# Optimization experiments

Measured on AMD Instinct MI355X. Metric: run time of the kernel, lower is better.

## Reference

```python
import jax, jax.numpy as jnp
import numpy as np

THRESH = 0.9   # config['thresh_cnn']
R = 2          # config['radius'] -> maxpool kernel 2R+1=5, stride 1, padding R


def setup_inputs() -> dict:
    key = jax.random.key(0)
    # [B=1, C=1, D=64, H=512, W=512]
    pred_vol = jax.random.uniform(key, (1, 1, 64, 512, 512), dtype=jnp.float32)
    return {"pred_vol": pred_vol}


def reference(pred_vol):
    # threshold: keep values > thresh, else 0
    pred_thresh = jnp.where(pred_vol > THRESH, pred_vol, 0.0)
    # 3D max-pool, kernel 2R+1, stride 1, padding R (torch pads with -inf for maxpool)
    k = 2 * R + 1
    mp = jax.lax.reduce_window(
        pred_thresh, -jnp.inf, jax.lax.max,
        window_dimensions=(1, 1, k, k, k),
        window_strides=(1, 1, 1, 1, 1),
        padding=[(0, 0), (0, 0), (R, R), (R, R), (R, R)],
    )
    # keep only strict local maxima of the thresholded volume
    conf_vol = jnp.where((mp > 0.0) & (mp == pred_thresh), mp, 0.0)
    return jnp.squeeze(conf_vol)  # [D, H, W] dense peak confidence map
```

## Files before the change

### kernel.cpp

```cpp
#include <hip/hip_runtime.h>


#define THRESH 0.9f

constexpr int D = 64, H = 512, W = 512;
constexpr int HW = H * W;
constexpr int TW = 64;
constexpr int TH = 16;
constexpr int DCHUNK = 16;
constexpr int HALO = 2;
constexpr int LROWS = TH + 2 * HALO;
constexpr int RAWQ  = TW / 4 + 2;
constexpr int RAW_S = RAWQ + 1;
constexpr int NS = DCHUNK + 2 * HALO;

typedef float floatx4 __attribute__((ext_vector_type(4)));

__device__ __forceinline__ void barrier_no_drain() {
    asm volatile("s_waitcnt lgkmcnt(0)\n\ts_barrier" ::: "memory");
}

__device__ __forceinline__ float4 max4(float4 a, float4 b) {
    return make_float4(fmaxf(a.x, b.x), fmaxf(a.y, b.y),
                       fmaxf(a.z, b.z), fmaxf(a.w, b.w));
}

__device__ __forceinline__ float4 wmax5s(float f2, float f3, float4 b,
                                         float f8, float f9) {
    const float f4 = b.x, f5 = b.y, f6 = b.z, f7 = b.w;
    const float m45 = fmaxf(f4, f5);
    const float m56 = fmaxf(f5, f6);
    const float m345 = fmaxf(f3, m45);
    const float m456 = fmaxf(f4, m56);
    const float m567 = fmaxf(m56, f7);
    const float m678 = fmaxf(fmaxf(f6, f7), f8);
    float4 r;
    r.x = fmaxf(fmaxf(f2, f6), m345);
    r.y = fmaxf(fmaxf(f3, f7), m456);
    r.z = fmaxf(fmaxf(f4, f8), m567);
    r.w = fmaxf(fmaxf(f5, f9), m678);
    return r;
}

__global__ __launch_bounds__(256)
void peak3d_kernel(const float* __restrict__ in, float* __restrict__ out) {
    __shared__ float4 raw[2][LROWS * RAW_S];

    const int tx = threadIdx.x;
    const int ty = threadIdx.y;
    const int tid = ty * 16 + tx;

    const int w0 = blockIdx.x * TW;
    const int h0 = blockIdx.y * TH;
    const int d0 = blockIdx.z * DCHUNK;

    const int q0 = tid;
    const int q1 = tid + 256;
    const int r0 = q0 / RAWQ, c0 = q0 % RAWQ;
    const int r1 = q1 / RAWQ, c1 = q1 % RAWQ;
    const int lds0 = r0 * RAW_S + c0;
    const int lds1 = r1 * RAW_S + c1;
    const int gh0 = h0 + r0 - HALO, gw0 = w0 + 4 * c0 - 4;
    const int gh1 = h0 + r1 - HALO, gw1 = w0 + 4 * c1 - 4;
    const bool has1 = (q1 < LROWS * RAWQ);
    const bool ib0 = (gh0 >= 0 && gh0 < H && gw0 >= 0 && gw0 < W);
    const bool ib1 = has1 && (gh1 >= 0 && gh1 < H && gw1 >= 0 && gw1 < W);
    const size_t off0 = ib0 ? ((size_t)gh0 * W + gw0) : 0;
    const size_t off1 = ib1 ? ((size_t)gh1 * W + gw1) : 0;

    const float4 zero4 = make_float4(0.f, 0.f, 0.f, 0.f);
    float4 win[5], cen[5];
#pragma unroll
    for (int k = 0; k < 5; ++k) { win[k] = zero4; cen[k] = zero4; }

    auto loadSlice = [&](int dd, float4& a, float4& b) {
        a = zero4; b = zero4;
        if (dd >= 0 && dd < D) {
            const size_t base = (size_t)dd * HW;
            if (ib0) a = *reinterpret_cast<const float4*>(in + base + off0);
            if (ib1) b = *reinterpret_cast<const float4*>(in + base + off1);
        }
    };

    float4 pfa[2], pfb[2];
    loadSlice(d0 - HALO + 0, pfa[0], pfb[0]);
    loadSlice(d0 - HALO + 1, pfa[1], pfb[1]);

    const int hcol = (tx == 0) ? 0 : (RAWQ - 1);

#pragma unroll
    for (int t = 0; t < NS; ++t) {
        const int buf = t & 1;

        raw[buf][lds0] = pfa[buf];
        if (has1) raw[buf][lds1] = pfb[buf];
        if (t + 2 < NS) loadSlice(d0 - HALO + t + 2, pfa[buf], pfb[buf]);

        barrier_no_drain();

        const float4* bp = &raw[buf][0];
        const float4 r0q = bp[(ty + 0) * RAW_S + (tx + 1)];
        const float4 r1q = bp[(ty + 1) * RAW_S + (tx + 1)];
        const float4 r2q = bp[(ty + 2) * RAW_S + (tx + 1)];
        const float4 r3q = bp[(ty + 3) * RAW_S + (tx + 1)];
        const float4 r4q = bp[(ty + 4) * RAW_S + (tx + 1)];
        const float4 hv = max4(max4(max4(r0q, r1q), max4(r3q, r4q)), r2q);

        const float4 e0 = bp[(ty + 0) * RAW_S + hcol];
        const float4 e1 = bp[(ty + 1) * RAW_S + hcol];
        const float4 e2 = bp[(ty + 2) * RAW_S + hcol];
        const float4 e3 = bp[(ty + 3) * RAW_S + hcol];
        const float4 e4 = bp[(ty + 4) * RAW_S + hcol];
        const float4 hq = max4(max4(max4(e0, e1), max4(e3, e4)), e2);

        float f2 = __shfl_up(hv.z, 1);
        float f3 = __shfl_up(hv.w, 1);
        float f8 = __shfl_down(hv.x, 1);
        float f9 = __shfl_down(hv.y, 1);
        if (tx == 0)  { f2 = hq.z; f3 = hq.w; }
        if (tx == 15) { f8 = hq.x; f9 = hq.y; }

        win[t % 5] = wmax5s(f2, f3, hv, f8, f9);
        cen[t % 5] = r2q;

        if (t >= 4) {
            const int dout = d0 + (t - 4);
            const float4 mp = max4(max4(max4(win[0], win[1]),
                                        max4(win[2], win[3])), win[4]);
            const float4 c = cen[(t + 3) % 5];
            floatx4 res;
            res.x = (c.x > THRESH && mp.x == c.x) ? c.x : 0.f;
            res.y = (c.y > THRESH && mp.y == c.y) ? c.y : 0.f;
            res.z = (c.z > THRESH && mp.z == c.z) ? c.z : 0.f;
            res.w = (c.w > THRESH && mp.w == c.w) ? c.w : 0.f;
            floatx4* op = reinterpret_cast<floatx4*>(
                out + (size_t)dout * HW + (size_t)(h0 + ty) * W + (w0 + 4 * tx));
            __builtin_nontemporal_store(res, op);
        }
    }
}

extern "C" void kernel_launch(void* const* d_in, const int* in_sizes, int n_in,
                              void* d_out, int out_size, void* d_ws, size_t ws_size,
                              hipStream_t stream) {
    const float* in = (const float*)d_in[0];
    float* out = (float*)d_out;
    dim3 grid(W / TW, H / TH, D / DCHUNK);
    dim3 block(16, 16, 1);
    hipLaunchKernelGGL(peak3d_kernel, grid, block, 0, stream, in, out);
}
```

Before: 116.6 us.

## Do W-direction max in registers before LDS, then vertical max from LDS

Each thread now loads three adjacent float4s per row (left, middle, right) straight from global memory and computes the 5-wide W max in registers. Only the W-maxed rows and the center values go to LDS, so the shuffles and separate halo-column reads are gone. The depth prefetch drops from two slices to one. This cuts LDS traffic and shuffle work but triples global load instructions, relying on cache hits for the overlapping neighbour reads, and raises register use.

```diff
diff --git a/kernel.cpp b/kernel.cpp
--- a/kernel.cpp
+++ b/kernel.cpp
@@ -10,8 +10,9 @@
 constexpr int DCHUNK = 16;
 constexpr int HALO = 2;
 constexpr int LROWS = TH + 2 * HALO;
-constexpr int RAWQ  = TW / 4 + 2;
-constexpr int RAW_S = RAWQ + 1;
+constexpr int WMC = 16;
+constexpr int WM_S = WMC + 1;
+constexpr int CEN_S = 17;
 constexpr int NS = DCHUNK + 2 * HALO;
 
 typedef float floatx4 __attribute__((ext_vector_type(4)));
@@ -25,9 +26,9 @@
                        fmaxf(a.z, b.z), fmaxf(a.w, b.w));
 }
 
-__device__ __forceinline__ float4 wmax5s(float f2, float f3, float4 b,
-                                         float f8, float f9) {
-    const float f4 = b.x, f5 = b.y, f6 = b.z, f7 = b.w;
+__device__ __forceinline__ float4 wmax5(float4 a, float4 b, float4 c) {
+    const float f2 = a.z, f3 = a.w, f4 = b.x, f5 = b.y, f6 = b.z, f7 = b.w;
+    const float f8 = c.x, f9 = c.y;
     const float m45 = fmaxf(f4, f5);
     const float m56 = fmaxf(f5, f6);
     const float m345 = fmaxf(f3, m45);
@@ -44,7 +45,8 @@
 
 __global__ __launch_bounds__(256)
 void peak3d_kernel(const float* __restrict__ in, float* __restrict__ out) {
-    __shared__ float4 raw[2][LROWS * RAW_S];
+    __shared__ float4 wm [2][LROWS * WM_S];
+    __shared__ float4 cen[2][TH * CEN_S];
 
     const int tx = threadIdx.x;
     const int ty = threadIdx.y;
@@ -54,80 +56,90 @@
     const int h0 = blockIdx.y * TH;
     const int d0 = blockIdx.z * DCHUNK;
 
-    const int q0 = tid;
-    const int q1 = tid + 256;
-    const int r0 = q0 / RAWQ, c0 = q0 % RAWQ;
-    const int r1 = q1 / RAWQ, c1 = q1 % RAWQ;
-    const int lds0 = r0 * RAW_S + c0;
-    const int lds1 = r1 * RAW_S + c1;
-    const int gh0 = h0 + r0 - HALO, gw0 = w0 + 4 * c0 - 4;
-    const int gh1 = h0 + r1 - HALO, gw1 = w0 + 4 * c1 - 4;
-    const bool has1 = (q1 < LROWS * RAWQ);
-    const bool ib0 = (gh0 >= 0 && gh0 < H && gw0 >= 0 && gw0 < W);
-    const bool ib1 = has1 && (gh1 >= 0 && gh1 < H && gw1 >= 0 && gw1 < W);
-    const size_t off0 = ib0 ? ((size_t)gh0 * W + gw0) : 0;
-    const size_t off1 = ib1 ? ((size_t)gh1 * W + gw1) : 0;
+    const int rA = tid >> 4, cA = (tid & 15) + 1;
+    const bool hasB = (tid < 64);
+    const int rB = 16 + (tid >> 4);
+    const int cB = cA;
+
+    const int ghA = h0 + rA - HALO;
+    const int ghB = h0 + rB - HALO;
+    const bool vAr_ = (unsigned)ghA < (unsigned)H;
+    const bool vBr_ = hasB && ((unsigned)ghB < (unsigned)H);
+    const int gwl = w0 + 4 * cA - 8;
+    const int gwm = w0 + 4 * cA - 4;
+    const int gwr = w0 + 4 * cA;
+    const bool vl = (unsigned)gwl < (unsigned)W;
+    const bool vr = (unsigned)gwr < (unsigned)W;
+    const size_t offAl = (size_t)(vAr_ ? ghA : 0) * W + (vl ? gwl : 0);
+    const size_t offAm = (size_t)(vAr_ ? ghA : 0) * W + gwm;
+    const size_t offAr = (size_t)(vAr_ ? ghA : 0) * W + (vr ? gwr : 0);
+    const size_t offBl = (size_t)(vBr_ ? ghB : 0) * W + (vl ? gwl : 0);
+    const size_t offBm = (size_t)(vBr_ ? ghB : 0) * W + gwm;
+    const size_t offBr = (size_t)(vBr_ ? ghB : 0) * W + (vr ? gwr : 0);
+    const bool vAl = vAr_ && vl, vAm = vAr_, vArr = vAr_ && vr;
+    const bool vBl = vBr_ && vl, vBm = vBr_, vBrr = vBr_ && vr;
 
     const float4 zero4 = make_float4(0.f, 0.f, 0.f, 0.f);
-    float4 win[5], cen[5];
+    float4 win[5], cen_r[3];
 #pragma unroll
-    for (int k = 0; k < 5; ++k) { win[k] = zero4; cen[k] = zero4; }
+    for (int k = 0; k < 5; ++k) win[k] = zero4;
+#pragma unroll
+    for (int k = 0; k < 3; ++k) cen_r[k] = zero4;
 
-    auto loadSlice = [&](int dd, float4& a, float4& b) {
-        a = zero4; b = zero4;
+    auto ld4 = [&](size_t off) {
+        return *reinterpret_cast<const float4*>(in + off);
+    };
+    auto loadStage = [&](int dd, float4* pf) {
+#pragma unroll
+        for (int i = 0; i < 6; ++i) pf[i] = zero4;
         if (dd >= 0 && dd < D) {
-            const size_t base = (size_t)dd * HW;
-            if (ib0) a = *reinterpret_cast<const float4*>(in + base + off0);
-            if (ib1) b = *reinterpret_cast<const float4*>(in + base + off1);
+            const size_t sb = (size_t)dd * HW;
+            if (vAl)  pf[0] = ld4(sb + offAl);
+            if (vAm)  pf[1] = ld4(sb + offAm);
+            if (vArr) pf[2] = ld4(sb + offAr);
+            if (vBl)  pf[3] = ld4(sb + offBl);
+            if (vBm)  pf[4] = ld4(sb + offBm);
+            if (vBrr) pf[5] = ld4(sb + offBr);
         }
     };
 
-    float4 pfa[2], pfb[2];
-    loadSlice(d0 - HALO + 0, pfa[0], pfb[0]);
-    loadSlice(d0 - HALO + 1, pfa[1], pfb[1]);
-
-    const int hcol = (tx == 0) ? 0 : (RAWQ - 1);
+    float4 pf[6];
+    loadStage(d0 - HALO, pf);
 
 #pragma unroll
     for (int t = 0; t < NS; ++t) {
         const int buf = t & 1;
 
-        raw[buf][lds0] = pfa[buf];
-        if (has1) raw[buf][lds1] = pfb[buf];
-        if (t + 2 < NS) loadSlice(d0 - HALO + t + 2, pfa[buf], pfb[buf]);
+        {
+            const float4 wA = wmax5(pf[0], pf[1], pf[2]);
+            wm[buf][rA * WM_S + (cA - 1)] = wA;
+            if (rA >= HALO)
+                cen[buf][(rA - HALO) * CEN_S + (cA - 1)] = pf[1];
+            if (hasB) {
+                const float4 wB = wmax5(pf[3], pf[4], pf[5]);
+                wm[buf][rB * WM_S + (cB - 1)] = wB;
+                if (rB <= TH + HALO - 1)
+                    cen[buf][(rB - HALO) * CEN_S + (cB - 1)] = pf[4];
+            }
+        }
+        if (t + 1 < NS) loadStage(d0 - HALO + t + 1, pf);
 
         barrier_no_drain();
 
-        const float4* bp = &raw[buf][0];
-        const float4 r0q = bp[(ty + 0) * RAW_S + (tx + 1)];
-        const float4 r1q = bp[(ty + 1) * RAW_S + (tx + 1)];
-        const float4 r2q = bp[(ty + 2) * RAW_S + (tx + 1)];
-        const float4 r3q = bp[(ty + 3) * RAW_S + (tx + 1)];
-        const float4 r4q = bp[(ty + 4) * RAW_S + (tx + 1)];
-        const float4 hv = max4(max4(max4(r0q, r1q), max4(r3q, r4q)), r2q);
-
-        const float4 e0 = bp[(ty + 0) * RAW_S + hcol];
-        const float4 e1 = bp[(ty + 1) * RAW_S + hcol];
-        const float4 e2 = bp[(ty + 2) * RAW_S + hcol];
-        const float4 e3 = bp[(ty + 3) * RAW_S + hcol];
-        const float4 e4 = bp[(ty + 4) * RAW_S + hcol];
-        const float4 hq = max4(max4(max4(e0, e1), max4(e3, e4)), e2);
-
-        float f2 = __shfl_up(hv.z, 1);
-        float f3 = __shfl_up(hv.w, 1);
-        float f8 = __shfl_down(hv.x, 1);
-        float f9 = __shfl_down(hv.y, 1);
-        if (tx == 0)  { f2 = hq.z; f3 = hq.w; }
-        if (tx == 15) { f8 = hq.x; f9 = hq.y; }
-
-        win[t % 5] = wmax5s(f2, f3, hv, f8, f9);
-        cen[t % 5] = r2q;
+        {
+            const float4* wp = &wm[buf][ty * WM_S + tx];
+            const float4 hv = max4(max4(max4(wp[0 * WM_S], wp[1 * WM_S]),
+                                        max4(wp[3 * WM_S], wp[4 * WM_S])),
+                                   wp[2 * WM_S]);
+            win[t % 5] = hv;
+            cen_r[t % 3] = cen[buf][ty * CEN_S + tx];
+        }
 
         if (t >= 4) {
             const int dout = d0 + (t - 4);
             const float4 mp = max4(max4(max4(win[0], win[1]),
                                         max4(win[2], win[3])), win[4]);
-            const float4 c = cen[(t + 3) % 5];
+            const float4 c = cen_r[(t + 1) % 3];
             floatx4 res;
             res.x = (c.x > THRESH && mp.x == c.x) ? c.x : 0.f;
             res.y = (c.y > THRESH && mp.y == c.y) ? c.y : 0.f;
```

Result: no change. 117.0 us (+0.4%).
